# Kernel tuning notes

Measured on AMD Instinct MI355X. Metric: run time of the kernel, lower is better.

Reference implementation:

```python
import jax, jax.numpy as jnp
import numpy as np

T, B, H, V, U = 64, 256, 256, 10000, 1024
LAMBDA_T = 0.1
LAMBDA_S = 100.0
DAY_SECS = 86400.0


def setup_inputs() -> dict:
    key = jax.random.key(0)
    ks = jax.random.split(key, 12)
    x = jax.random.randint(ks[0], (T, B), 0, V)
    # timestamps: increasing along the sequence dim per user, span one week
    t = jnp.sort(jax.random.uniform(ks[1], (T, B)) * (7.0 * DAY_SECS), axis=0)
    s = jax.random.uniform(ks[2], (T, B, 2)) * 0.1  # lat/lon-like coords
    h = jnp.zeros((B, H), dtype=jnp.float32)
    active_user = jax.random.randint(ks[3], (B,), 0, U)
    poi_emb = jax.random.normal(ks[4], (V, H), dtype=jnp.float32) * 0.02
    user_emb = jax.random.normal(ks[5], (U, H), dtype=jnp.float32) * 0.02
    gru_wx = jax.random.normal(ks[6], (H, 3 * H), dtype=jnp.float32) / np.sqrt(H)
    gru_wh = jax.random.normal(ks[7], (H, 3 * H), dtype=jnp.float32) / np.sqrt(H)
    gru_b = jnp.zeros((3 * H,), dtype=jnp.float32)
    fc_w = jax.random.normal(ks[8], (2 * H, V), dtype=jnp.float32) / np.sqrt(2 * H)
    fc_b = jnp.zeros((V,), dtype=jnp.float32)
    return {"x": x, "t": t, "s": s, "h": h, "active_user": active_user,
            "poi_emb": poi_emb, "user_emb": user_emb,
            "gru_wx": gru_wx, "gru_wh": gru_wh, "gru_b": gru_b,
            "fc_w": fc_w, "fc_b": fc_b}


def _gru(x_seq, h0, wx, wh, b):
    # x_seq: [T, B, H], h0: [B, H]
    def step(hprev, xt):
        gx = xt @ wx + b          # [B, 3H]
        gh = hprev @ wh           # [B, 3H]
        gx_r, gx_z, gx_n = jnp.split(gx, 3, axis=-1)
        gh_r, gh_z, gh_n = jnp.split(gh, 3, axis=-1)
        r = jax.nn.sigmoid(gx_r + gh_r)
        z = jax.nn.sigmoid(gx_z + gh_z)
        n = jnp.tanh(gx_n + r * gh_n)
        hnew = (1.0 - z) * n + z * hprev
        return hnew, hnew
    h_final, out = jax.lax.scan(step, h0, x_seq)
    return out, h_final


def reference(x, t, s, h, active_user, poi_emb, user_emb,
              gru_wx, gru_wh, gru_b, fc_w, fc_b):
    # POI embedding lookup: [T, B, H]
    x_emb = poi_emb[x]
    # recurrent encoder over the sequence (stands in for GMSR/RNN unit)
    out, h_final = _gru(x_emb, h, gru_wx, gru_wh, gru_b)
    # pairwise spatio-temporal weights, causal (j <= i)
    dist_t = t[:, None, :] - t[None, :, :]                       # [T, T, B]
    dist_s = jnp.linalg.norm(s[:, None] - s[None, :], axis=-1)   # [T, T, B]
    f_t = 0.5 * (jnp.cos(dist_t * (2.0 * jnp.pi / DAY_SECS)) + 1.0) \
          * jnp.exp(-(dist_t / DAY_SECS) * LAMBDA_T)
    f_s = jnp.exp(-dist_s * LAMBDA_S)
    w = f_t * f_s + 1e-10                                         # [T, T, B]
    causal = jnp.tril(jnp.ones((T, T), dtype=w.dtype))            # j <= i
    w = w * causal[:, :, None]
    sum_w = jnp.sum(w, axis=1)                                    # [T, B]
    out_w = jnp.einsum('ijb,jbh->ibh', w, out) / sum_w[:, :, None]
    # user embedding concat + final projection to POI vocab
    p_u = user_emb[active_user]                                   # [B, H]
    out_pu = jnp.concatenate(
        [out_w, jnp.broadcast_to(p_u[None], (T, B, H))], axis=-1)  # [T, B, 2H]
    y_linear = out_pu @ fc_w + fc_b                               # [T, B, V]
    return y_linear, h_final
```

## Files before the change

### kernel.cpp

```cpp
#include <hip/hip_runtime.h>
#include <math.h>

#define Tn 64
#define Bn 256
#define Hn 256
#define Vn 10000

__global__ __launch_bounds__(256) void k_transpose_wh(const float* __restrict__ wh,
                                                      float* __restrict__ whT) {
    int n = blockIdx.x;
    int k = threadIdx.x;
    whT[n * 256 + k] = wh[k * 768 + n];
}

template <int MODE>
__global__ __launch_bounds__(256) void k_gemm(const float* __restrict__ Abase,
                                              const int* __restrict__ gidx,
                                              const float* __restrict__ Bg,
                                              const float* __restrict__ bias,
                                              float* __restrict__ C,
                                              int N, int ldb, int koff) {
    __shared__ float As[64][64];
    __shared__ float Bs[64][64];

    const int tid = threadIdx.x;
    const int m0 = blockIdx.y * 64;
    const int n0 = blockIdx.x * 64;

    const int m_l = tid & 63;
    const int kq = tid >> 6;
    long arow;
    if (MODE == 2) arow = (long)(m0 + m_l);
    else           arow = (long)gidx[m0 + m_l];
    const float* Ap = Abase + arow * 256;

    const int nc = tid & 15;
    const int kr0 = tid >> 4;

    const int ty = tid >> 4, tx = tid & 15;

    float acc[4][4];
#pragma unroll
    for (int r = 0; r < 4; ++r)
#pragma unroll
        for (int c = 0; c < 4; ++c) acc[r][c] = 0.f;

    for (int k0 = 0; k0 < 256; k0 += 64) {
#pragma unroll
        for (int i = 0; i < 4; ++i) {
            int kc = kq + i * 4;
            float4 a4 = *(const float4*)(Ap + k0 + kc * 4);
            As[kc * 4 + 0][m_l] = a4.x;
            As[kc * 4 + 1][m_l] = a4.y;
            As[kc * 4 + 2][m_l] = a4.z;
            As[kc * 4 + 3][m_l] = a4.w;
        }
#pragma unroll
        for (int i = 0; i < 4; ++i) {
            int kr = kr0 + i * 16;
            int col = n0 + nc * 4;
            float4 b4;
            if (MODE == 0 || col < N) {
                b4 = *(const float4*)(Bg + (long)(koff + k0 + kr) * ldb + col);
            } else {
                b4 = make_float4(0.f, 0.f, 0.f, 0.f);
            }
            *(float4*)&Bs[kr][nc * 4] = b4;
        }
        __syncthreads();
#pragma unroll
        for (int kk = 0; kk < 64; ++kk) {
            float4 a4 = *(const float4*)&As[kk][ty * 4];
            float4 b4 = *(const float4*)&Bs[kk][tx * 4];
            acc[0][0] += a4.x * b4.x; acc[0][1] += a4.x * b4.y;
            acc[0][2] += a4.x * b4.z; acc[0][3] += a4.x * b4.w;
            acc[1][0] += a4.y * b4.x; acc[1][1] += a4.y * b4.y;
            acc[1][2] += a4.y * b4.z; acc[1][3] += a4.y * b4.w;
            acc[2][0] += a4.z * b4.x; acc[2][1] += a4.z * b4.y;
            acc[2][2] += a4.z * b4.z; acc[2][3] += a4.z * b4.w;
            acc[3][0] += a4.w * b4.x; acc[3][1] += a4.w * b4.y;
            acc[3][2] += a4.w * b4.z; acc[3][3] += a4.w * b4.w;
        }
        __syncthreads();
    }

#pragma unroll
    for (int r = 0; r < 4; ++r) {
        int m = m0 + ty * 4 + r;
#pragma unroll
        for (int c = 0; c < 4; ++c) {
            int n = n0 + tx * 4 + c;
            if (MODE == 0) {
                C[(long)m * N + n] = acc[r][c] + bias[n];
            } else if (MODE == 1) {
                if (n < N) C[(long)m * N + n] = acc[r][c] + bias[n];
            } else {
                if (n < N) C[(long)m * N + n] = acc[r][c] + bias[(long)(m & 255) * N + n];
            }
        }
    }
}

__global__ __launch_bounds__(256) void k_gru_step(const float* __restrict__ gx,
                                                  const float* __restrict__ hprev,
                                                  const float* __restrict__ whT,
                                                  float* __restrict__ hout) {
    __shared__ float hs[16][260];
    __shared__ float ws[48][260];

    const int tid = threadIdx.x;
    const int h0 = blockIdx.x * 16;
    const int b0 = blockIdx.y * 16;

#pragma unroll
    for (int i = 0; i < 4; ++i) {
        int idx = tid + i * 256;
        int row = idx >> 6, c4 = idx & 63;
        *(float4*)&hs[row][c4 * 4] = *(const float4*)(hprev + (b0 + row) * 256 + c4 * 4);
    }
#pragma unroll
    for (int i = 0; i < 12; ++i) {
        int idx = tid + i * 256;
        int row = idx >> 6, c4 = idx & 63;
        int g = row >> 4, hh = row & 15;
        *(float4*)&ws[row][c4 * 4] = *(const float4*)(whT + (g * 256 + h0 + hh) * 256 + c4 * 4);
    }
    __syncthreads();

    const int tb = tid >> 4, th = tid & 15;
    float ra = 0.f, za = 0.f, na = 0.f;
#pragma unroll 16
    for (int k4 = 0; k4 < 64; ++k4) {
        float4 h4 = *(const float4*)&hs[tb][k4 * 4];
        float4 wr = *(const float4*)&ws[th][k4 * 4];
        float4 wz = *(const float4*)&ws[16 + th][k4 * 4];
        float4 wn = *(const float4*)&ws[32 + th][k4 * 4];
        ra += h4.x * wr.x + h4.y * wr.y + h4.z * wr.z + h4.w * wr.w;
        za += h4.x * wz.x + h4.y * wz.y + h4.z * wz.z + h4.w * wz.w;
        na += h4.x * wn.x + h4.y * wn.y + h4.z * wn.z + h4.w * wn.w;
    }
    const int b = b0 + tb, h = h0 + th;
    float gxr = gx[b * 768 + h];
    float gxz = gx[b * 768 + 256 + h];
    float gxn = gx[b * 768 + 512 + h];
    float hp = hs[tb][h];
    float r = 1.f / (1.f + expf(-(gxr + ra)));
    float z = 1.f / (1.f + expf(-(gxz + za)));
    float nn = tanhf(gxn + r * na);
    hout[b * 256 + h] = (1.f - z) * nn + z * hp;
}

__global__ __launch_bounds__(256) void k_stw(const float* __restrict__ t_in,
                                             const float* __restrict__ s_in,
                                             const float* __restrict__ OUT,
                                             float* __restrict__ OUTW) {
    __shared__ float tl[64];
    __shared__ float sl[64][2];
    __shared__ float w[64][64];
    __shared__ float swinv[64];
    __shared__ float outc[16][256];

    const int b = blockIdx.x;
    const int tid = threadIdx.x;

    if (tid < 64) tl[tid] = t_in[tid * Bn + b];
    if (tid < 128) {
        int i = tid >> 1, c = tid & 1;
        sl[i][c] = s_in[(i * Bn + b) * 2 + c];
    }
    __syncthreads();

    const float TWO_PI_OVER_DAY = 6.283185307179586f / 86400.0f;
    const float LT_OVER_DAY = 0.1f / 86400.0f;
#pragma unroll
    for (int e = tid; e < 4096; e += 256) {
        int i = e >> 6, j = e & 63;
        float v = 0.f;
        if (j <= i) {
            float dt = tl[i] - tl[j];
            float dx = sl[i][0] - sl[j][0];
            float dy = sl[i][1] - sl[j][1];
            float dsd = sqrtf(dx * dx + dy * dy);
            float ft = 0.5f * (cosf(dt * TWO_PI_OVER_DAY) + 1.f) * expf(-dt * LT_OVER_DAY);
            float fs = expf(-dsd * 100.0f);
            v = ft * fs + 1e-10f;
        }
        w[i][j] = v;
    }
    __syncthreads();
    if (tid < 64) {
        float s = 0.f;
        for (int j = 0; j <= tid; ++j) s += w[tid][j];
        swinv[tid] = 1.f / s;
    }
    __syncthreads();

    for (int it = 0; it < 4; ++it) {
        float accs[16];
#pragma unroll
        for (int q = 0; q < 16; ++q) accs[q] = 0.f;
        for (int jt = 0; jt <= it; ++jt) {
            __syncthreads();
#pragma unroll
            for (int i2 = 0; i2 < 4; ++i2) {
                int idx = tid + i2 * 256;
                int jr = idx >> 6, c4 = idx & 63;
                *(float4*)&outc[jr][c4 * 4] =
                    *(const float4*)(OUT + ((long)(jt * 16 + jr) * Bn + b) * Hn + c4 * 4);
            }
            __syncthreads();
#pragma unroll
            for (int i_l = 0; i_l < 16; ++i_l) {
                int i = it * 16 + i_l;
                int jmax = (jt < it) ? 15 : i_l;
                float a = accs[i_l];
                for (int j_l = 0; j_l <= jmax; ++j_l)
                    a += w[i][jt * 16 + j_l] * outc[j_l][tid];
                accs[i_l] = a;
            }
        }
#pragma unroll
        for (int i_l = 0; i_l < 16; ++i_l) {
            int i = it * 16 + i_l;
            OUTW[((long)i * Bn + b) * Hn + tid] = accs[i_l] * swinv[i];
        }
    }
}

__global__ __launch_bounds__(256) void k_copy4(const float* __restrict__ src,
                                               float* __restrict__ dst, int n4) {
    int i = blockIdx.x * 256 + threadIdx.x;
    if (i < n4) ((float4*)dst)[i] = ((const float4*)src)[i];
}

extern "C" void kernel_launch(void* const* d_in, const int* in_sizes, int n_in,
                              void* d_out, int out_size, void* d_ws, size_t ws_size,
                              hipStream_t stream) {
    const int*   x     = (const int*)  d_in[0];
    const float* t_in  = (const float*)d_in[1];
    const float* s_in  = (const float*)d_in[2];
    const float* h0    = (const float*)d_in[3];
    const int*   auser = (const int*)  d_in[4];
    const float* poi   = (const float*)d_in[5];
    const float* uemb  = (const float*)d_in[6];
    const float* wx    = (const float*)d_in[7];
    const float* wh    = (const float*)d_in[8];
    const float* gb    = (const float*)d_in[9];
    const float* fcw   = (const float*)d_in[10];
    const float* fcb   = (const float*)d_in[11];

    float* GX   = (float*)d_ws;
    float* OUT  = GX + (long)Tn * Bn * 768;
    float* OUTW = OUT + (long)Tn * Bn * Hn;
    float* UC   = OUTW + (long)Tn * Bn * Hn;
    float* WHT  = UC + (long)Bn * Vn;

    float* y    = (float*)d_out;
    float* hfin = y + (long)Tn * Bn * Vn;

    k_transpose_wh<<<768, 256, 0, stream>>>(wh, WHT);

    k_gemm<0><<<dim3(12, 256), 256, 0, stream>>>(poi, x, wx, gb, GX, 768, 768, 0);

    k_gemm<1><<<dim3(157, 4), 256, 0, stream>>>(uemb, auser, fcw, fcb, UC, Vn, Vn, 256);

    for (int t = 0; t < Tn; ++t) {
        const float* hp = (t == 0) ? h0 : (OUT + (long)(t - 1) * Bn * Hn);
        k_gru_step<<<dim3(16, 16), 256, 0, stream>>>(GX + (long)t * Bn * 768, hp, WHT,
                                                     OUT + (long)t * Bn * Hn);
    }
    k_copy4<<<64, 256, 0, stream>>>(OUT + (long)(Tn - 1) * Bn * Hn, hfin, (Bn * Hn) / 4);

    k_stw<<<256, 256, 0, stream>>>(t_in, s_in, OUT, OUTW);

    k_gemm<2><<<dim3(157, 256), 256, 0, stream>>>(OUTW, nullptr, fcw, UC, y, Vn, Vn, 0);
}
```

Before: 2.410 ms.

## Use bf16 MFMA GEMMs and a cooperative persistent GRU kernel

Result: slower. 3.376 ms (+40.1%).

```diff
diff --git a/kernel.cpp b/kernel.cpp
--- a/kernel.cpp
+++ b/kernel.cpp
@@ -1,10 +1,23 @@
 #include <hip/hip_runtime.h>
+#include <hip/hip_cooperative_groups.h>
 #include <math.h>
+
+namespace cg = cooperative_groups;
 
 #define Tn 64
 #define Bn 256
 #define Hn 256
 #define Vn 10000
+#define NPAD 10112
+
+typedef __attribute__((ext_vector_type(8))) short short8;
+typedef __attribute__((ext_vector_type(4))) float f32x4;
+
+__device__ inline unsigned short f2bf(float f) {
+    unsigned int u = __float_as_uint(f);
+    unsigned int r = (u + 0x7fff + ((u >> 16) & 1)) >> 16;
+    return (unsigned short)r;
+}
 
 __global__ __launch_bounds__(256) void k_transpose_wh(const float* __restrict__ wh,
                                                       float* __restrict__ whT) {
@@ -13,30 +26,135 @@
     whT[n * 256 + k] = wh[k * 768 + n];
 }
 
-template <int MODE>
-__global__ __launch_bounds__(256) void k_gemm(const float* __restrict__ Abase,
+__global__ __launch_bounds__(256) void k_transpose_bf16(const float* __restrict__ src, int ld,
+                                                        int nlimit, unsigned short* __restrict__ dst) {
+    __shared__ float tl[64][65];
+    const int n0 = blockIdx.x * 64, k0 = blockIdx.y * 64;
+    const int tid = threadIdx.x;
+    const int c = tid & 63, r0 = tid >> 6;
+#pragma unroll
+    for (int i = 0; i < 16; ++i) {
+        int r = r0 + i * 4;
+        tl[r][c] = (n0 + c < nlimit) ? src[(long)(k0 + r) * ld + n0 + c] : 0.f;
+    }
+    __syncthreads();
+#pragma unroll
+    for (int i = 0; i < 16; ++i) {
+        int nr = r0 + i * 4;
+        dst[(long)(n0 + nr) * 256 + k0 + c] = f2bf(tl[c][nr]);
+    }
+}
+
+__global__ __launch_bounds__(256) void k_f2bf4(const float* __restrict__ src,
+                                               unsigned short* __restrict__ dst, int n4) {
+    int i = blockIdx.x * 256 + threadIdx.x;
+    if (i < n4) {
+        float4 v = ((const float4*)src)[i];
+        ushort4 o;
+        o.x = f2bf(v.x); o.y = f2bf(v.y); o.z = f2bf(v.z); o.w = f2bf(v.w);
+        ((ushort4*)dst)[i] = o;
+    }
+}
+
+template <int GATHER>
+__global__ __launch_bounds__(256) void k_mfma(const unsigned short* __restrict__ Atab,
                                               const int* __restrict__ gidx,
-                                              const float* __restrict__ Bg,
-                                              const float* __restrict__ bias,
+                                              const unsigned short* __restrict__ Bt,
+                                              const float* __restrict__ biasN,
+                                              const float* __restrict__ biasMN,
                                               float* __restrict__ C,
-                                              int N, int ldb, int koff) {
+                                              int N, int Nlimit) {
+    __shared__ __align__(16) unsigned short Al[128 * 32];
+    __shared__ __align__(16) unsigned short Bl[128 * 32];
+
+    const int tid = threadIdx.x;
+    const int wave = tid >> 6, lane = tid & 63;
+    const int m0 = blockIdx.y * 128, n0 = blockIdx.x * 128;
+
+    const int c0 = wave * 64 + lane;
+    const int c1 = 256 + c0;
+    long arow0, arow1;
+    if (GATHER) { arow0 = gidx[m0 + (c0 >> 2)]; arow1 = gidx[m0 + (c1 >> 2)]; }
+    else        { arow0 = m0 + (c0 >> 2);       arow1 = m0 + (c1 >> 2); }
+    const unsigned short* Ap0 = Atab + arow0 * 256 + (c0 & 3) * 8;
+    const unsigned short* Ap1 = Atab + arow1 * 256 + (c1 & 3) * 8;
+    const unsigned short* Bp0 = Bt + (long)(n0 + (c0 >> 2)) * 256 + (c0 & 3) * 8;
+    const unsigned short* Bp1 = Bt + (long)(n0 + (c1 >> 2)) * 256 + (c1 & 3) * 8;
+
+    const int fr = lane & 15;
+    const int kq = lane >> 4;
+    const int wm = wave >> 1, wn = wave & 1;
+    const int aoff = (wm * 64 + fr) * 32 + kq * 8;
+    const int boff = (wn * 64 + fr) * 32 + kq * 8;
+
+    f32x4 acc[4][4];
+#pragma unroll
+    for (int i = 0; i < 4; ++i)
+#pragma unroll
+        for (int j = 0; j < 4; ++j) acc[i][j] = (f32x4){0.f, 0.f, 0.f, 0.f};
+
+    for (int k0 = 0; k0 < 256; k0 += 32) {
+        __builtin_amdgcn_global_load_lds(
+            (const __attribute__((address_space(1))) void*)(Ap0 + k0),
+            (__attribute__((address_space(3))) void*)(Al + wave * 512), 16, 0, 0);
+        __builtin_amdgcn_global_load_lds(
+            (const __attribute__((address_space(1))) void*)(Ap1 + k0),
+            (__attribute__((address_space(3))) void*)(Al + 2048 + wave * 512), 16, 0, 0);
+        __builtin_amdgcn_global_load_lds(
+            (const __attribute__((address_space(1))) void*)(Bp0 + k0),
+            (__attribute__((address_space(3))) void*)(Bl + wave * 512), 16, 0, 0);
+        __builtin_amdgcn_global_load_lds(
+            (const __attribute__((address_space(1))) void*)(Bp1 + k0),
+            (__attribute__((address_space(3))) void*)(Bl + 2048 + wave * 512), 16, 0, 0);
+        __syncthreads();
+
+        short8 af[4], bf[4];
+#pragma unroll
+        for (int i = 0; i < 4; ++i) af[i] = *(const short8*)(const void*)(Al + aoff + i * 512);
+#pragma unroll
+        for (int j = 0; j < 4; ++j) bf[j] = *(const short8*)(const void*)(Bl + boff + j * 512);
+#pragma unroll
+        for (int i = 0; i < 4; ++i)
+#pragma unroll
+            for (int j = 0; j < 4; ++j)
+                acc[i][j] = __builtin_amdgcn_mfma_f32_16x16x32_bf16(af[i], bf[j], acc[i][j], 0, 0, 0);
+        __syncthreads();
+    }
+
+#pragma unroll
+    for (int i = 0; i < 4; ++i) {
+#pragma unroll
+        for (int j = 0; j < 4; ++j) {
+            int n = n0 + wn * 64 + j * 16 + fr;
+            if (!GATHER && n >= Nlimit) continue;
+#pragma unroll
+            for (int q = 0; q < 4; ++q) {
+                int m = m0 + wm * 64 + i * 16 + kq * 4 + q;
+                float v = acc[i][j][q];
+                v += GATHER ? biasN[n] : biasMN[(long)(m & 255) * N + n];
+                C[(long)m * N + n] = v;
+            }
+        }
+    }
+}
+
+__global__ __launch_bounds__(256) void k_gemm_uc(const float* __restrict__ Abase,
+                                                 const int* __restrict__ gidx,
+                                                 const float* __restrict__ Bg,
+                                                 const float* __restrict__ bias,
+                                                 float* __restrict__ C,
+                                                 int N, int ldb, int koff) {
     __shared__ float As[64][64];
     __shared__ float Bs[64][64];
-
     const int tid = threadIdx.x;
     const int m0 = blockIdx.y * 64;
     const int n0 = blockIdx.x * 64;
-
     const int m_l = tid & 63;
     const int kq = tid >> 6;
-    long arow;
-    if (MODE == 2) arow = (long)(m0 + m_l);
-    else           arow = (long)gidx[m0 + m_l];
+    long arow = (long)gidx[m0 + m_l];
     const float* Ap = Abase + arow * 256;
-
     const int nc = tid & 15;
     const int kr0 = tid >> 4;
-
     const int ty = tid >> 4, tx = tid & 15;
 
     float acc[4][4];
@@ -60,11 +178,8 @@
             int kr = kr0 + i * 16;
             int col = n0 + nc * 4;
             float4 b4;
-            if (MODE == 0 || col < N) {
-                b4 = *(const float4*)(Bg + (long)(koff + k0 + kr) * ldb + col);
-            } else {
-                b4 = make_float4(0.f, 0.f, 0.f, 0.f);
-            }
+            if (col < N) b4 = *(const float4*)(Bg + (long)(koff + k0 + kr) * ldb + col);
+            else b4 = make_float4(0.f, 0.f, 0.f, 0.f);
             *(float4*)&Bs[kr][nc * 4] = b4;
         }
         __syncthreads();
@@ -83,77 +198,78 @@
         }
         __syncthreads();
     }
-
 #pragma unroll
     for (int r = 0; r < 4; ++r) {
         int m = m0 + ty * 4 + r;
 #pragma unroll
         for (int c = 0; c < 4; ++c) {
             int n = n0 + tx * 4 + c;
-            if (MODE == 0) {
-                C[(long)m * N + n] = acc[r][c] + bias[n];
-            } else if (MODE == 1) {
-                if (n < N) C[(long)m * N + n] = acc[r][c] + bias[n];
-            } else {
-                if (n < N) C[(long)m * N + n] = acc[r][c] + bias[(long)(m & 255) * N + n];
-            }
-        }
-    }
-}
-
-__global__ __launch_bounds__(256) void k_gru_step(const float* __restrict__ gx,
-                                                  const float* __restrict__ hprev,
-                                                  const float* __restrict__ whT,
-                                                  float* __restrict__ hout) {
+            if (n < N) C[(long)m * N + n] = acc[r][c] + bias[n];
+        }
+    }
+}
+
+__global__ __launch_bounds__(256, 1) void k_gru_all(const float* __restrict__ GX,
+                                                    const float* __restrict__ h0,
+                                                    const float* __restrict__ whT,
+                                                    float* __restrict__ OUT) {
+    cg::grid_group grid = cg::this_grid();
+    __shared__ float ws[48][260];
     __shared__ float hs[16][260];
-    __shared__ float ws[48][260];
 
     const int tid = threadIdx.x;
-    const int h0 = blockIdx.x * 16;
-    const int b0 = blockIdx.y * 16;
-
-#pragma unroll
-    for (int i = 0; i < 4; ++i) {
-        int idx = tid + i * 256;
-        int row = idx >> 6, c4 = idx & 63;
-        *(float4*)&hs[row][c4 * 4] = *(const float4*)(hprev + (b0 + row) * 256 + c4 * 4);
-    }
+    const int hg = blockIdx.x & 15, bg = blockIdx.x >> 4;
+    const int h0c = hg * 16, b0 = bg * 16;
+
 #pragma unroll
     for (int i = 0; i < 12; ++i) {
         int idx = tid + i * 256;
         int row = idx >> 6, c4 = idx & 63;
         int g = row >> 4, hh = row & 15;
-        *(float4*)&ws[row][c4 * 4] = *(const float4*)(whT + (g * 256 + h0 + hh) * 256 + c4 * 4);
-    }
-    __syncthreads();
+        *(float4*)&ws[row][c4 * 4] = *(const float4*)(whT + (g * 256 + h0c + hh) * 256 + c4 * 4);
+    }
 
     const int tb = tid >> 4, th = tid & 15;
-    float ra = 0.f, za = 0.f, na = 0.f;
+    const int b = b0 + tb, h = h0c + th;
+
+    for (int t = 0; t < Tn; ++t) {
+        const float* hp = t ? (OUT + (long)(t - 1) * (Bn * Hn)) : h0;
+#pragma unroll
+        for (int i = 0; i < 4; ++i) {
+            int idx = tid + i * 256;
+            int row = idx >> 6, c4 = idx & 63;
+            *(float4*)&hs[row][c4 * 4] = *(const float4*)(hp + (b0 + row) * 256 + c4 * 4);
+        }
+        __syncthreads();
+
+        float ra = 0.f, za = 0.f, na = 0.f;
 #pragma unroll 16
-    for (int k4 = 0; k4 < 64; ++k4) {
-        float4 h4 = *(const float4*)&hs[tb][k4 * 4];
-        float4 wr = *(const float4*)&ws[th][k4 * 4];
-        float4 wz = *(const float4*)&ws[16 + th][k4 * 4];
-        float4 wn = *(const float4*)&ws[32 + th][k4 * 4];
-        ra += h4.x * wr.x + h4.y * wr.y + h4.z * wr.z + h4.w * wr.w;
-        za += h4.x * wz.x + h4.y * wz.y + h4.z * wz.z + h4.w * wz.w;
-        na += h4.x * wn.x + h4.y * wn.y + h4.z * wn.z + h4.w * wn.w;
-    }
-    const int b = b0 + tb, h = h0 + th;
-    float gxr = gx[b * 768 + h];
-    float gxz = gx[b * 768 + 256 + h];
-    float gxn = gx[b * 768 + 512 + h];
-    float hp = hs[tb][h];
-    float r = 1.f / (1.f + expf(-(gxr + ra)));
-    float z = 1.f / (1.f + expf(-(gxz + za)));
-    float nn = tanhf(gxn + r * na);
-    hout[b * 256 + h] = (1.f - z) * nn + z * hp;
+        for (int k4 = 0; k4 < 64; ++k4) {
+            float4 h4 = *(const float4*)&hs[tb][k4 * 4];
+            float4 wr = *(const float4*)&ws[th][k4 * 4];
+            float4 wz = *(const float4*)&ws[16 + th][k4 * 4];
+            float4 wn = *(const float4*)&ws[32 + th][k4 * 4];
+            ra += h4.x * wr.x + h4.y * wr.y + h4.z * wr.z + h4.w * wr.w;
+            za += h4.x * wz.x + h4.y * wz.y + h4.z * wz.z + h4.w * wz.w;
+            na += h4.x * wn.x + h4.y * wn.y + h4.z * wn.z + h4.w * wn.w;
+        }
+        long gxb = ((long)t * Bn + b) * 768;
+        float gxr = GX[gxb + h];
+        float gxz = GX[gxb + 256 + h];
+        float gxn = GX[gxb + 512 + h];
+        float hpv = hs[tb][h];
+        float r = 1.f / (1.f + expf(-(gxr + ra)));
+        float z = 1.f / (1.f + expf(-(gxz + za)));
+        float nn = tanhf(gxn + r * na);
+        OUT[(long)t * (Bn * Hn) + b * 256 + h] = (1.f - z) * nn + z * hpv;
+        grid.sync();
+    }
 }
 
 __global__ __launch_bounds__(256) void k_stw(const float* __restrict__ t_in,
                                              const float* __restrict__ s_in,
                                              const float* __restrict__ OUT,
-                                             float* __restrict__ OUTW) {
+                                             unsigned short* __restrict__ OUTW) {
     __shared__ float tl[64];
     __shared__ float sl[64][2];
     __shared__ float w[64][64];
@@ -222,7 +338,7 @@
 #pragma unroll
         for (int i_l = 0; i_l < 16; ++i_l) {
             int i = it * 16 + i_l;
-            OUTW[((long)i * Bn + b) * Hn + tid] = accs[i_l] * swinv[i];
+            OUTW[((long)i * Bn + b) * Hn + tid] = f2bf(accs[i_l] * swinv[i]);
         }
     }
 }
@@ -249,29 +365,37 @@
     const float* fcw   = (const float*)d_in[10];
     const float* fcb   = (const float*)d_in[11];
 
-    float* GX   = (float*)d_ws;
-    float* OUT  = GX + (long)Tn * Bn * 768;
-    float* OUTW = OUT + (long)Tn * Bn * Hn;
-    float* UC   = OUTW + (long)Tn * Bn * Hn;
-    float* WHT  = UC + (long)Bn * Vn;
+    char* w = (char*)d_ws;
+    float*          GX   = (float*)w;
+    unsigned short* OUTW = (unsigned short*)w;
+    float*          OUT  = (float*)(w + 50331648);
+    float*          UC   = (float*)(w + 67108864);
+    float*          WHT  = (float*)(w + 77348864);
+    unsigned short* POIB = (unsigned short*)(w + 78135296);
+    unsigned short* WXT  = (unsigned short*)(w + 83255296);
+    unsigned short* FCWT = (unsigned short*)(w + 83648512);
 
     float* y    = (float*)d_out;
     float* hfin = y + (long)Tn * Bn * Vn;
 
     k_transpose_wh<<<768, 256, 0, stream>>>(wh, WHT);
-
-    k_gemm<0><<<dim3(12, 256), 256, 0, stream>>>(poi, x, wx, gb, GX, 768, 768, 0);
-
-    k_gemm<1><<<dim3(157, 4), 256, 0, stream>>>(uemb, auser, fcw, fcb, UC, Vn, Vn, 256);
-
-    for (int t = 0; t < Tn; ++t) {
-        const float* hp = (t == 0) ? h0 : (OUT + (long)(t - 1) * Bn * Hn);
-        k_gru_step<<<dim3(16, 16), 256, 0, stream>>>(GX + (long)t * Bn * 768, hp, WHT,
-                                                     OUT + (long)t * Bn * Hn);
+    k_f2bf4<<<2500, 256, 0, stream>>>(poi, POIB, (Vn * Hn) / 4);
+    k_transpose_bf16<<<dim3(12, 4), 256, 0, stream>>>(wx, 768, 768, WXT);
+    k_transpose_bf16<<<dim3(NPAD / 64, 4), 256, 0, stream>>>(fcw, Vn, Vn, FCWT);
+
+    k_mfma<1><<<dim3(6, 128), 256, 0, stream>>>(POIB, x, WXT, gb, nullptr, GX, 768, 768);
+
+    k_gemm_uc<<<dim3(157, 4), 256, 0, stream>>>(uemb, auser, fcw, fcb, UC, Vn, Vn, 256);
+
+    {
+        const float* gxp = GX; const float* h0p = h0; const float* whtp = WHT; float* outp = OUT;
+        void* gargs[] = {(void*)&gxp, (void*)&h0p, (void*)&whtp, (void*)&outp};
+        hipLaunchCooperativeKernel(reinterpret_cast<void*>(&k_gru_all),
+                                   dim3(256), dim3(256), gargs, 0, stream);
     }
     k_copy4<<<64, 256, 0, stream>>>(OUT + (long)(Tn - 1) * Bn * Hn, hfin, (Bn * Hn) / 4);
 
     k_stw<<<256, 256, 0, stream>>>(t_in, s_in, OUT, OUTW);
 
-    k_gemm<2><<<dim3(157, 256), 256, 0, stream>>>(OUTW, nullptr, fcw, UC, y, Vn, Vn, 0);
-}
+    k_mfma<0><<<dim3(NPAD / 128, 128), 256, 0, stream>>>(OUTW, nullptr, FCWT, nullptr, UC, y, Vn, Vn);
+}
```
